# Kernel optimization log

Measured on AMD Instinct MI355X. Metric: run time of the kernel, lower is better.

## Reference

```python
import itertools
import jax, jax.numpy as jnp
import numpy as np

GRID = 16384      # self.shape = (GRID,)
LAYERS = 8        # num_layers
SPAN = 2          # span = (2,)
K = 2 * SPAN + 1  # kernel size = 5 (ninputs)
NPOS = 2 ** K     # 32 possible boolean input combos
BATCH = 32
M = 4096          # x width; GRID % M == 0
STRIDE = GRID // M

# bitmask: all 2^K boolean input combinations, shape (NPOS, K)
_BITMASK = jnp.asarray(list(itertools.product(range(2), repeat=K)), dtype=jnp.float32)


def setup_inputs() -> dict:
    key = jax.random.key(0)
    k1, k2 = jax.random.split(key)
    x = jax.random.uniform(k1, (BATCH, M), dtype=jnp.float32)
    toggle_gates = jax.random.uniform(k2, (LAYERS, NPOS, GRID), dtype=jnp.float32)
    return {"x": x, "toggle_gates": toggle_gates}


def _convolve(state):
    # torch convolve(): offsets 0..K-1 via wrap-around roll, then spatial roll by
    # -SPAN to center the window -> neighbor n+i-SPAN (mod GRID) at kernel idx i.
    # jnp.roll(state, SPAN - i) gives out[:, n] = state[:, n + i - SPAN mod GRID].
    return jnp.stack([jnp.roll(state, SPAN - i, axis=1) for i in range(K)], axis=-1)  # (B, N, K)


def reference(x, toggle_gates):
    tw = jax.nn.sigmoid(toggle_gates)  # (L, NPOS, N)
    # embed(): scatter x evenly into the grid, rest is scratch (zeros)
    state = jnp.zeros((x.shape[0], GRID), dtype=x.dtype).at[:, ::STRIDE].set(x)

    def step(s, tw_layer):
        conv = _convolve(s)  # (B, N, K)
        # weight[c, b, n] = prod_i (1 - |bitmask[c, i] - conv[b, n, i]|)
        w = jnp.prod(1.0 - jnp.abs(_BITMASK[:, None, None, :] - conv[None]), axis=-1)  # (C, B, N)
        new = jnp.clip(jnp.einsum('cbn,cn->bn', w, tw_layer), 0.0, 1.0)
        return new, None

    state, _ = jax.lax.scan(step, state, tw)
    # forward returns state[slices] = state[:, ::STRIDE]
    return state[:, ::STRIDE]
```

## Files before the change

### kernel.cpp

```cpp
#include <hip/hip_runtime.h>

#define GRID_N 16384
#define NLAYERS 8
#define NPOS 32
#define BATCH 32
#define MW 4096
#define TILE 32
#define HALO 16
#define WBUF 64
#define ROWP 36

typedef float f2 __attribute__((ext_vector_type(2)));

__global__ __launch_bounds__(256, 2) void ASIC_44186623541335_kernel(
    const float* __restrict__ x,
    const float* __restrict__ tg,
    float* __restrict__ out)
{
    __shared__ __align__(16) float st[WBUF][ROWP];
    __shared__ __align__(16) float twl[4][WBUF][ROWP];

    const int tid = threadIdx.x;
    const int tx  = tid & 63;
    const int ty  = tid >> 6;
    const int c0  = 8 * ty;
    const int start = blockIdx.x * TILE;
    const int gcol  = (start - HALO + tx) & (GRID_N - 1);

    float pf[32];
    #pragma unroll
    for (int l4 = 0; l4 < 4; ++l4)
        #pragma unroll
        for (int k = 0; k < 8; ++k)
            pf[l4 * 8 + k] = tg[((size_t)l4 * NPOS + c0 + k) * GRID_N + gcol];

    for (int f = tid; f < WBUF * BATCH; f += 256) {
        const int b = f >> 6;
        const int j = f & 63;
        const int g = (start - HALO + j) & (GRID_N - 1);
        st[j][b] = ((g & 3) == 0) ? x[b * MW + (g >> 2)] : 0.0f;
    }

    #pragma unroll
    for (int l4 = 0; l4 < 4; ++l4) {
        #pragma unroll
        for (int h4 = 0; h4 < 2; ++h4) {
            float4 sg;
            sg.x = __builtin_amdgcn_rcpf(1.0f + __expf(-pf[l4 * 8 + 4 * h4 + 0]));
            sg.y = __builtin_amdgcn_rcpf(1.0f + __expf(-pf[l4 * 8 + 4 * h4 + 1]));
            sg.z = __builtin_amdgcn_rcpf(1.0f + __expf(-pf[l4 * 8 + 4 * h4 + 2]));
            sg.w = __builtin_amdgcn_rcpf(1.0f + __expf(-pf[l4 * 8 + 4 * h4 + 3]));
            *(float4*)&twl[l4][tx][c0 + 4 * h4] = sg;
        }
    }
    #pragma unroll
    for (int l4 = 0; l4 < 4; ++l4)
        #pragma unroll
        for (int k = 0; k < 8; ++k)
            pf[l4 * 8 + k] = tg[((size_t)(4 + l4) * NPOS + c0 + k) * GRID_N + gcol];
    __syncthreads();

    for (int l = 0; l < NLAYERS; ++l) {
        const int h     = 2 * (NLAYERS - 1 - l);
        const int ncols = TILE + 2 * h;
        const int j     = (HALO - h) + tx;

        if (tx < ncols) {
            float tw[32];
            #pragma unroll
            for (int k = 0; k < 8; ++k) {
                const float4 q = *(const float4*)&twl[l & 3][j][4 * k];
                tw[4 * k]     = q.x; tw[4 * k + 1] = q.y;
                tw[4 * k + 2] = q.z; tw[4 * k + 3] = q.w;
            }
            float d0[16];
            #pragma unroll
            for (int r = 0; r < 16; ++r) d0[r] = tw[16 + r] - tw[r];

            float4 A[5][2];
            #pragma unroll
            for (int o = 0; o < 5; ++o) {
                A[o][0] = *(const float4*)&st[j - 2 + o][c0];
                A[o][1] = *(const float4*)&st[j - 2 + o][c0 + 4];
            }

            float4 res[2];
            #pragma unroll
            for (int q = 0; q < 4; ++q) {
                const int hi = q >> 1, lo = (q & 1) * 2;
                const f2 s0 = { ((const float*)&A[0][hi])[lo], ((const float*)&A[0][hi])[lo + 1] };
                const f2 s1 = { ((const float*)&A[1][hi])[lo], ((const float*)&A[1][hi])[lo + 1] };
                const f2 s2 = { ((const float*)&A[2][hi])[lo], ((const float*)&A[2][hi])[lo + 1] };
                const f2 s3 = { ((const float*)&A[3][hi])[lo], ((const float*)&A[3][hi])[lo + 1] };
                const f2 s4 = { ((const float*)&A[4][hi])[lo], ((const float*)&A[4][hi])[lo + 1] };

                f2 u[16];
                #pragma unroll
                for (int r = 0; r < 16; ++r)
                    u[r] = __builtin_elementwise_fma(s0, (f2)d0[r], (f2)tw[r]);
                #pragma unroll
                for (int r = 0; r < 8; ++r)
                    u[r] = __builtin_elementwise_fma(s1, u[8 + r] - u[r], u[r]);
                #pragma unroll
                for (int r = 0; r < 4; ++r)
                    u[r] = __builtin_elementwise_fma(s2, u[4 + r] - u[r], u[r]);
                #pragma unroll
                for (int r = 0; r < 2; ++r)
                    u[r] = __builtin_elementwise_fma(s3, u[2 + r] - u[r], u[r]);
                f2 rv = __builtin_elementwise_fma(s4, u[1] - u[0], u[0]);
                rv = __builtin_elementwise_min(__builtin_elementwise_max(rv, (f2)0.0f), (f2)1.0f);
                ((float*)&res[hi])[lo]     = rv.x;
                ((float*)&res[hi])[lo + 1] = rv.y;
            }
            *(float4*)&st[j][c0]     = res[0];
            *(float4*)&st[j][c0 + 4] = res[1];
        }
        __builtin_amdgcn_wave_barrier();

        if (l == 3) {
            __syncthreads();
            #pragma unroll
            for (int l4 = 0; l4 < 4; ++l4) {
                #pragma unroll
                for (int h4 = 0; h4 < 2; ++h4) {
                    float4 sg;
                    sg.x = __builtin_amdgcn_rcpf(1.0f + __expf(-pf[l4 * 8 + 4 * h4 + 0]));
                    sg.y = __builtin_amdgcn_rcpf(1.0f + __expf(-pf[l4 * 8 + 4 * h4 + 1]));
                    sg.z = __builtin_amdgcn_rcpf(1.0f + __expf(-pf[l4 * 8 + 4 * h4 + 2]));
                    sg.w = __builtin_amdgcn_rcpf(1.0f + __expf(-pf[l4 * 8 + 4 * h4 + 3]));
                    *(float4*)&twl[l4][tx][c0 + 4 * h4] = sg;
                }
            }
            __syncthreads();
        }
    }

    __syncthreads();
    {
        const int c4 = tid & 7;
        const int b  = tid >> 3;
        out[b * MW + (start >> 2) + c4] = st[HALO + 4 * c4][b];
    }
}

extern "C" void kernel_launch(void* const* d_in, const int* in_sizes, int n_in,
                              void* d_out, int out_size, void* d_ws, size_t ws_size,
                              hipStream_t stream) {
    const float* x  = (const float*)d_in[0];
    const float* tg = (const float*)d_in[1];
    float* out = (float*)d_out;
    ASIC_44186623541335_kernel<<<GRID_N / TILE, 256, 0, stream>>>(x, tg, out);
}
```

Baseline: 82.68 us.

## Keep automaton state in registers and exchange neighbors via DPP wave shifts

The per-layer grid state moves from a shared-memory tile into per-lane registers. The five-neighbor window now comes from DPP wave_shr1/wave_shl1 lane shifts instead of LDS reads and writes, which removes those LDS accesses and the wave barrier each layer. The initial embed and the final output write go straight between global memory and registers. Every lane now computes all 64 columns each layer. Lanes at the wave edges get zeros from the shifts, which relies on the 16-column halo covering the window shrinkage over the 8 layers.

```diff
diff --git a/kernel.cpp b/kernel.cpp
--- a/kernel.cpp
+++ b/kernel.cpp
@@ -12,12 +12,22 @@
 
 typedef float f2 __attribute__((ext_vector_type(2)));
 
+__device__ __forceinline__ float dpp_shr1(float v) {
+    return __builtin_bit_cast(float, __builtin_amdgcn_update_dpp(
+        0, __builtin_bit_cast(int, v), 0x138, 0xF, 0xF, true));
+}
+__device__ __forceinline__ float dpp_shl1(float v) {
+    return __builtin_bit_cast(float, __builtin_amdgcn_update_dpp(
+        0, __builtin_bit_cast(int, v), 0x130, 0xF, 0xF, true));
+}
+__device__ __forceinline__ f2 shr1(f2 v) { f2 r; r.x = dpp_shr1(v.x); r.y = dpp_shr1(v.y); return r; }
+__device__ __forceinline__ f2 shl1(f2 v) { f2 r; r.x = dpp_shl1(v.x); r.y = dpp_shl1(v.y); return r; }
+
 __global__ __launch_bounds__(256, 2) void ASIC_44186623541335_kernel(
     const float* __restrict__ x,
     const float* __restrict__ tg,
     float* __restrict__ out)
 {
-    __shared__ __align__(16) float st[WBUF][ROWP];
     __shared__ __align__(16) float twl[4][WBUF][ROWP];
 
     const int tid = threadIdx.x;
@@ -34,11 +44,19 @@
         for (int k = 0; k < 8; ++k)
             pf[l4 * 8 + k] = tg[((size_t)l4 * NPOS + c0 + k) * GRID_N + gcol];
 
-    for (int f = tid; f < WBUF * BATCH; f += 256) {
-        const int b = f >> 6;
-        const int j = f & 63;
-        const int g = (start - HALO + j) & (GRID_N - 1);
-        st[j][b] = ((g & 3) == 0) ? x[b * MW + (g >> 2)] : 0.0f;
+    f2 S[4];
+    {
+        const bool on = (gcol & 3) == 0;
+        const int  m  = gcol >> 2;
+        #pragma unroll
+        for (int q = 0; q < 4; ++q) {
+            f2 v = {0.0f, 0.0f};
+            if (on) {
+                v.x = x[(c0 + 2 * q)     * MW + m];
+                v.y = x[(c0 + 2 * q + 1) * MW + m];
+            }
+            S[q] = v;
+        }
     }
 
     #pragma unroll
@@ -61,61 +79,45 @@
     __syncthreads();
 
     for (int l = 0; l < NLAYERS; ++l) {
-        const int h     = 2 * (NLAYERS - 1 - l);
-        const int ncols = TILE + 2 * h;
-        const int j     = (HALO - h) + tx;
+        float tw[32];
+        #pragma unroll
+        for (int k = 0; k < 8; ++k) {
+            const float4 q = *(const float4*)&twl[l & 3][tx][4 * k];
+            tw[4 * k]     = q.x; tw[4 * k + 1] = q.y;
+            tw[4 * k + 2] = q.z; tw[4 * k + 3] = q.w;
+        }
+        float d0[16];
+        #pragma unroll
+        for (int r = 0; r < 16; ++r) d0[r] = tw[16 + r] - tw[r];
 
-        if (tx < ncols) {
-            float tw[32];
+        f2 s0v[4], s1v[4], s3v[4], s4v[4];
+        #pragma unroll
+        for (int q = 0; q < 4; ++q) {
+            s1v[q] = shr1(S[q]);
+            s0v[q] = shr1(s1v[q]);
+            s3v[q] = shl1(S[q]);
+            s4v[q] = shl1(s3v[q]);
+        }
+
+        #pragma unroll
+        for (int q = 0; q < 4; ++q) {
+            f2 u[16];
             #pragma unroll
-            for (int k = 0; k < 8; ++k) {
-                const float4 q = *(const float4*)&twl[l & 3][j][4 * k];
-                tw[4 * k]     = q.x; tw[4 * k + 1] = q.y;
-                tw[4 * k + 2] = q.z; tw[4 * k + 3] = q.w;
-            }
-            float d0[16];
+            for (int r = 0; r < 16; ++r)
+                u[r] = __builtin_elementwise_fma(s0v[q], (f2)d0[r], (f2)tw[r]);
             #pragma unroll
-            for (int r = 0; r < 16; ++r) d0[r] = tw[16 + r] - tw[r];
-
-            float4 A[5][2];
+            for (int r = 0; r < 8; ++r)
+                u[r] = __builtin_elementwise_fma(s1v[q], u[8 + r] - u[r], u[r]);
             #pragma unroll
-            for (int o = 0; o < 5; ++o) {
-                A[o][0] = *(const float4*)&st[j - 2 + o][c0];
-                A[o][1] = *(const float4*)&st[j - 2 + o][c0 + 4];
-            }
-
-            float4 res[2];
+            for (int r = 0; r < 4; ++r)
+                u[r] = __builtin_elementwise_fma(S[q], u[4 + r] - u[r], u[r]);
             #pragma unroll
-            for (int q = 0; q < 4; ++q) {
-                const int hi = q >> 1, lo = (q & 1) * 2;
-                const f2 s0 = { ((const float*)&A[0][hi])[lo], ((const float*)&A[0][hi])[lo + 1] };
-                const f2 s1 = { ((const float*)&A[1][hi])[lo], ((const float*)&A[1][hi])[lo + 1] };
-                const f2 s2 = { ((const float*)&A[2][hi])[lo], ((const float*)&A[2][hi])[lo + 1] };
-                const f2 s3 = { ((const float*)&A[3][hi])[lo], ((const float*)&A[3][hi])[lo + 1] };
-                const f2 s4 = { ((const float*)&A[4][hi])[lo], ((const float*)&A[4][hi])[lo + 1] };
-
-                f2 u[16];
-                #pragma unroll
-                for (int r = 0; r < 16; ++r)
-                    u[r] = __builtin_elementwise_fma(s0, (f2)d0[r], (f2)tw[r]);
-                #pragma unroll
-                for (int r = 0; r < 8; ++r)
-                    u[r] = __builtin_elementwise_fma(s1, u[8 + r] - u[r], u[r]);
-                #pragma unroll
-                for (int r = 0; r < 4; ++r)
-                    u[r] = __builtin_elementwise_fma(s2, u[4 + r] - u[r], u[r]);
-                #pragma unroll
-                for (int r = 0; r < 2; ++r)
-                    u[r] = __builtin_elementwise_fma(s3, u[2 + r] - u[r], u[r]);
-                f2 rv = __builtin_elementwise_fma(s4, u[1] - u[0], u[0]);
-                rv = __builtin_elementwise_min(__builtin_elementwise_max(rv, (f2)0.0f), (f2)1.0f);
-                ((float*)&res[hi])[lo]     = rv.x;
-                ((float*)&res[hi])[lo + 1] = rv.y;
-            }
-            *(float4*)&st[j][c0]     = res[0];
-            *(float4*)&st[j][c0 + 4] = res[1];
+            for (int r = 0; r < 2; ++r)
+                u[r] = __builtin_elementwise_fma(s3v[q], u[2 + r] - u[r], u[r]);
+            f2 rv = __builtin_elementwise_fma(s4v[q], u[1] - u[0], u[0]);
+            rv = __builtin_elementwise_min(__builtin_elementwise_max(rv, (f2)0.0f), (f2)1.0f);
+            S[q] = rv;
         }
-        __builtin_amdgcn_wave_barrier();
 
         if (l == 3) {
             __syncthreads();
@@ -135,11 +137,14 @@
         }
     }
 
-    __syncthreads();
-    {
-        const int c4 = tid & 7;
-        const int b  = tid >> 3;
-        out[b * MW + (start >> 2) + c4] = st[HALO + 4 * c4][b];
+    const int rel = tx - HALO;
+    if (rel >= 0 && rel < TILE && (rel & 3) == 0) {
+        const int m = (start >> 2) + (rel >> 2);
+        #pragma unroll
+        for (int q = 0; q < 4; ++q) {
+            out[(c0 + 2 * q)     * MW + m] = S[q].x;
+            out[(c0 + 2 * q + 1) * MW + m] = S[q].y;
+        }
     }
 }
 
```

Result: faster. 80.81 us (-2.3%).
